# Kernel optimization log

Hardware: AMD Instinct MI355X
Metric: run time of the kernel (lower is better)

## Reference

```python
import jax, jax.numpy as jnp
import numpy as np

E = 65536            # total entities (flattened batch*history*slots)
ENTITY_SIZE = 256
NUM_SPECIES, NUM_ABILITIES, NUM_ITEMS, NUM_ACTIONS = 512, 128, 256, 512
# feature layout (column index in entity row)
SPECIES, ABILITY, ITEM = 0, 1, 2
SCALAR_FEATS = list(range(3, 16))   # level..fainted
SCALAR_MAX = [101, 2, 2, 32, 3, 8, 16, 2, 2, 2, 8, 4, 2]
BOOST_FEATS = list(range(16, 23))   # 7 boosts
BOOST_MAX = 13
VOL0, VOL8 = 23, 31                 # 9 uint16 volatile words
TC0, TC1 = 32, 33                   # 2 uint16 typechange words
MOVE0 = 34                          # 4 move-id tokens
NUM_FEATS = 38
HP_RATIO = 6
CONCAT_DIM = 512 + 128 + 256 + sum(SCALAR_MAX) + 7 * BOOST_MAX + 9 * 16 + 2 * 16 + 1  # = 1348

MAXES = np.ones(NUM_FEATS, dtype=np.int32)
MAXES[SPECIES], MAXES[ABILITY], MAXES[ITEM] = NUM_SPECIES, NUM_ABILITIES, NUM_ITEMS
for f, m in zip(SCALAR_FEATS, SCALAR_MAX):
    MAXES[f] = m
for f in BOOST_FEATS:
    MAXES[f] = BOOST_MAX
MAXES[VOL0:VOL8 + 1] = 65536
MAXES[TC0:TC1 + 1] = 65536
MAXES[MOVE0:MOVE0 + 4] = NUM_ACTIONS


def bits16(x):
    # x int32 [..., k] -> float bits [..., k*16]
    b = (x[..., None] >> jnp.arange(16, dtype=jnp.int32)) & 1
    return b.astype(jnp.float32).reshape(*x.shape[:-1], -1)


def setup_inputs() -> dict:
    key = jax.random.key(0)
    ks = jax.random.split(key, 12)
    u = jax.random.uniform(ks[0], (E, NUM_FEATS))
    entity = (u * jnp.asarray(MAXES, dtype=jnp.float32)).astype(jnp.int32)
    s = 0.02
    return {
        'entity': entity,
        'species_tbl': jax.random.normal(ks[1], (NUM_SPECIES, 512), jnp.float32) * s,
        'ability_tbl': jax.random.normal(ks[2], (NUM_ABILITIES, 128), jnp.float32) * s,
        'item_tbl': jax.random.normal(ks[3], (NUM_ITEMS, 256), jnp.float32) * s,
        'species_emb': jax.random.normal(ks[4], (NUM_SPECIES, ENTITY_SIZE), jnp.float32) * s,
        'ability_emb': jax.random.normal(ks[5], (NUM_ABILITIES, ENTITY_SIZE), jnp.float32) * s,
        'item_emb': jax.random.normal(ks[6], (NUM_ITEMS, ENTITY_SIZE), jnp.float32) * s,
        'actions_emb': jax.random.normal(ks[7], (NUM_ACTIONS, ENTITY_SIZE), jnp.float32) * s,
        'agg_w': jax.random.normal(ks[8], (CONCAT_DIM, ENTITY_SIZE), jnp.float32) * s,
        'agg_b': jnp.zeros((ENTITY_SIZE,), jnp.float32),
        'mlp_w': jax.random.normal(ks[9], (ENTITY_SIZE, ENTITY_SIZE), jnp.float32) * s,
        'mlp_b': jnp.zeros((ENTITY_SIZE,), jnp.float32),
    }


def reference(entity, species_tbl, ability_tbl, item_tbl, species_emb, ability_emb,
              item_emb, actions_emb, agg_w, agg_b, mlp_w, mlp_b):
    sp, ab, it = entity[:, SPECIES], entity[:, ABILITY], entity[:, ITEM]
    # pretrained one-hot / feature-table gathers
    enc = [species_tbl[sp], ability_tbl[ab], item_tbl[it]]
    # small scalar one-hots
    enc += [jax.nn.one_hot(entity[:, f], m, dtype=jnp.float32)
            for f, m in zip(SCALAR_FEATS, SCALAR_MAX)]
    # boost one-hots
    enc += [jax.nn.one_hot(entity[:, f], BOOST_MAX, dtype=jnp.float32) for f in BOOST_FEATS]
    # hex/binary encodings of volatile + typechange words
    enc.append(bits16(entity[:, VOL0:VOL8 + 1]))       # [E,144]
    enc.append(bits16(entity[:, TC0:TC1 + 1]))         # [E,32]
    # continuous feature (hp ratio)
    enc.append((entity[:, HP_RATIO].astype(jnp.float32) / 31.0)[:, None])
    concat = jnp.concatenate(enc, axis=-1)             # [E,1348]
    emb_sum = (species_emb[sp] + ability_emb[ab] + item_emb[it]
               + actions_emb[entity[:, MOVE0]] + actions_emb[entity[:, MOVE0 + 1]]
               + actions_emb[entity[:, MOVE0 + 2]] + actions_emb[entity[:, MOVE0 + 3]])
    x = concat @ agg_w + agg_b + emb_sum               # SumEmbeddings
    x = jax.nn.relu(x) @ mlp_w + mlp_b                 # MLP((entity_size,))
    mask = jnp.logical_and(sp != 0, sp != 1)           # not NULL / not PAD
    return jnp.where(mask[:, None], x, 0.0)
```

## Files before the change

### kernel.cpp

```cpp
#include <hip/hip_runtime.h>

#define NFEAT 38

typedef __attribute__((ext_vector_type(8))) short bf16x8;
typedef __attribute__((ext_vector_type(4))) float f32x4;
typedef __attribute__((ext_vector_type(2))) float f32x2;
typedef __attribute__((ext_vector_type(4))) unsigned int u32x4;

#define R_SP   0
#define R_AB   512
#define R_IT   640
#define R_T1   896
#define R_T2   1300
#define R_T3   1428
#define R_T4   1452
#define R_T5   1484
#define R_T6   1548
#define R_T7   1717
#define R_T8   1886
#define R_T9   2055
#define R_ACT  2068
#define NROWS  2580

#define B_FUSED  0
#define B_WMLP   112
#define B_WBITS  176
#define B_MERGED 224
#define B_IDXS   645
#define NB_PREP  709

__device__ __forceinline__ unsigned short f2bf(float f) {
    unsigned int u = __float_as_uint(f);
    u += 0x7fffu + ((u >> 16) & 1u);
    return (unsigned short)(u >> 16);
}

__device__ __forceinline__ unsigned int cvt_pk_bf16(float lo, float hi) {
    unsigned int r;
    asm("v_cvt_pk_bf16_f32 %0, %1, %2" : "=v"(r) : "v"(lo), "v"(hi));
    return r;
}

__global__ __launch_bounds__(1024) void k_prep(
    const float* __restrict__ sp_tbl, const float* __restrict__ ab_tbl,
    const float* __restrict__ it_tbl, const float* __restrict__ sp_emb,
    const float* __restrict__ ab_emb, const float* __restrict__ it_emb,
    const float* __restrict__ act_emb, const float* __restrict__ agg_w,
    const float* __restrict__ agg_b,  const float* __restrict__ mlp_w,
    const int* __restrict__ ent,
    unsigned short* __restrict__ tbl, unsigned short* __restrict__ wfrag,
    unsigned short* __restrict__ wbits, unsigned int* __restrict__ ridx)
{
    __shared__ float rowbuf[8 * 513];
    __shared__ float part[8][4][256];
    int blk = blockIdx.x, t = threadIdx.x, c = t & 255;
#define W(x) agg_w[(size_t)(x) * 256 + c]

    if (blk < B_WMLP) {
        int r0 = blk << 3;
        const float* src; const float* emb; int len, wbase, ls; bool add_b;
        if (r0 < 512)      { src = sp_tbl + (size_t)r0 * 512;           emb = sp_emb + (size_t)r0 * 256;           len = 512; ls = 9; wbase = 0;   add_b = true;  }
        else if (r0 < 640) { int q = r0 - 512; src = ab_tbl + (size_t)q * 128; emb = ab_emb + (size_t)q * 256; len = 128; ls = 7; wbase = 512; add_b = false; }
        else               { int q = r0 - 640; src = it_tbl + (size_t)q * 256; emb = it_emb + (size_t)q * 256; len = 256; ls = 8; wbase = 640; add_b = false; }
        int tot = len << 3;
        for (int i = t; i < tot; i += 1024)
            rowbuf[(i >> ls) * (len + 1) + (i & (len - 1))] = src[i];
        __syncthreads();
        int kq   = t >> 8;
        int len4 = len >> 2;
        int kbeg = kq * len4, kend = kbeg + len4;
        float a[8] = {0.f, 0.f, 0.f, 0.f, 0.f, 0.f, 0.f, 0.f};
        #pragma unroll 4
        for (int k = kbeg; k < kend; ++k) {
            float w = W(wbase + k);
            #pragma unroll
            for (int r = 0; r < 8; ++r) a[r] += rowbuf[r * (len + 1) + k] * w;
        }
        #pragma unroll
        for (int r = 0; r < 8; ++r) part[r][kq][c] = a[r];
        __syncthreads();
        int rr = t >> 8;
        #pragma unroll
        for (int h = 0; h < 2; ++h) {
            int row = rr + h * 4;
            float s = part[row][0][c] + part[row][1][c] + part[row][2][c] + part[row][3][c]
                    + emb[row * 256 + c] + (add_b ? agg_b[c] : 0.f);
            tbl[(size_t)(r0 + row) * 256 + c] = f2bf(s);
        }
        return;
    }
    if (blk < B_WBITS) {
        int idx = ((blk - B_WMLP) << 10) + t;
        int j   = idx & 7;
        int fl  = (idx >> 3) & 63;
        int k0g = (idx >> 9) & 7;
        int nt  = idx >> 12;
        int k   = k0g * 32 + (fl >> 4) * 8 + j;
        int col = nt * 16 + (fl & 15);
        wfrag[idx] = f2bf(mlp_w[(size_t)k * 256 + col]);
        return;
    }
    if (blk < B_MERGED) {
        int idx = ((blk - B_WBITS) << 10) + t;
        int j   = idx & 7;
        int ln  = (idx >> 3) & 63;
        int r2  = idx >> 9;
        int kt  = r2 % 6;
        int nt  = r2 / 6;
        int k   = kt * 32 + ((ln >> 4) << 3) + j;
        int col = (nt << 4) + (ln & 15);
        float v = (k < 176) ? agg_w[(size_t)(1171 + k) * 256 + col] : 0.f;
        wbits[idx] = f2bf(v);
        return;
    }
    if (blk < B_IDXS) {
        int r = ((blk - B_MERGED) << 2) + (t >> 8);
        int row; float acc;
        if (r < 404)       { int f3 = r >> 2, f4 = (r >> 1) & 1, f5 = r & 1;
                             acc = W(896 + f3) + W(997 + f4) + W(999 + f5); row = R_T1 + r; }
        else if (r < 532)  { int i = r - 404; int f6 = i >> 2, f11 = (i >> 1) & 1, f12 = i & 1;
                             acc = W(1001 + f6) + (float)f6 * (1.f / 31.f) * W(1347)
                                 + W(1062 + f11) + W(1064 + f12); row = R_T2 + i; }
        else if (r < 556)  { int i = r - 532; acc = W(1033 + (i >> 3)) + W(1036 + (i & 7)); row = R_T3 + i; }
        else if (r < 588)  { int i = r - 556; acc = W(1044 + (i >> 1)) + W(1060 + (i & 1)); row = R_T4 + i; }
        else if (r < 652)  { int i = r - 588; acc = W(1066 + (i >> 3)) + W(1074 + ((i >> 1) & 3)) + W(1078 + (i & 1)); row = R_T5 + i; }
        else if (r < 821)  { int i = r - 652; acc = W(1080 + i / 13) + W(1093 + i % 13); row = R_T6 + i; }
        else if (r < 990)  { int i = r - 821; acc = W(1106 + i / 13) + W(1119 + i % 13); row = R_T7 + i; }
        else if (r < 1159) { int i = r - 990; acc = W(1132 + i / 13) + W(1145 + i % 13); row = R_T8 + i; }
        else if (r < 1172) { int i = r - 1159; acc = W(1158 + i); row = R_T9 + i; }
        else               { int i = r - 1172; acc = act_emb[(size_t)i * 256 + c]; row = R_ACT + i; }
        tbl[(size_t)row * 256 + c] = f2bf(acc);
        return;
    }
    {
        int e = ((blk - B_IDXS) << 10) + t;
        size_t bb = (size_t)e * (NFEAT * 4);
        const uint4* wp = reinterpret_cast<const uint4*>(
            reinterpret_cast<const char*>(ent) + (bb & ~(size_t)15));
        uint4 q0 = wp[0], q1 = wp[1], q2 = wp[2], q3 = wp[3], q4 = wp[4];
        uint4 q5 = wp[5], q6 = wp[6], q7 = wp[7], q8 = wp[8], q9 = wp[9];
        unsigned int v[40] = {q0.x,q0.y,q0.z,q0.w, q1.x,q1.y,q1.z,q1.w,
                              q2.x,q2.y,q2.z,q2.w, q3.x,q3.y,q3.z,q3.w,
                              q4.x,q4.y,q4.z,q4.w, q5.x,q5.y,q5.z,q5.w,
                              q6.x,q6.y,q6.z,q6.w, q7.x,q7.y,q7.z,q7.w,
                              q8.x,q8.y,q8.z,q8.w, q9.x,q9.y,q9.z,q9.w};
        int f[NFEAT];
        if (e & 1) {
            #pragma unroll
            for (int i = 0; i < NFEAT; ++i) f[i] = (int)v[i + 2];
        } else {
            #pragma unroll
            for (int i = 0; i < NFEAT; ++i) f[i] = (int)v[i];
        }
        int rw[16];
        rw[0]  = f[0];
        rw[1]  = R_AB + f[1];
        rw[2]  = R_IT + f[2];
        rw[3]  = R_T1 + f[3] * 4 + f[4] * 2 + f[5];
        rw[4]  = R_T2 + f[6] * 4 + f[11] * 2 + f[12];
        rw[5]  = R_T3 + f[7] * 8 + f[8];
        rw[6]  = R_T4 + f[9] * 2 + f[10];
        rw[7]  = R_T5 + f[13] * 8 + f[14] * 2 + f[15];
        rw[8]  = R_T6 + f[16] * 13 + f[17];
        rw[9]  = R_T7 + f[18] * 13 + f[19];
        rw[10] = R_T8 + f[20] * 13 + f[21];
        rw[11] = R_T9 + f[22];
        rw[12] = R_ACT + f[34];
        rw[13] = R_ACT + f[35];
        rw[14] = R_ACT + f[36];
        rw[15] = R_ACT + f[37];
        unsigned int p[16];
        #pragma unroll
        for (int i = 0; i < 8; ++i)
            p[i] = (unsigned int)rw[2 * i] | ((unsigned int)rw[2 * i + 1] << 16);
        #pragma unroll
        for (int i = 0; i < 5; ++i)
            p[8 + i] = (unsigned int)(f[23 + 2 * i] & 0xffff) | ((unsigned int)f[24 + 2 * i] << 16);
        p[13] = (unsigned int)(f[33] & 0xffff);
        p[14] = 0; p[15] = 0;
        uint4* dst = reinterpret_cast<uint4*>(ridx + (size_t)e * 16);
        dst[0] = make_uint4(p[0], p[1], p[2], p[3]);
        dst[1] = make_uint4(p[4], p[5], p[6], p[7]);
        dst[2] = make_uint4(p[8], p[9], p[10], p[11]);
        dst[3] = make_uint4(p[12], p[13], p[14], p[15]);
    }
#undef W
}

__global__ __launch_bounds__(512, 4) void k_fused_em(
    const unsigned int* __restrict__ ridx, const unsigned short* __restrict__ tbl,
    const unsigned short* __restrict__ wfrag, const unsigned short* __restrict__ wbits,
    const float* __restrict__ mlp_b, float* __restrict__ out)
{
    __shared__ unsigned short xw[64 * 256];
    __shared__ unsigned int bitw[64 * 6];
    __shared__ unsigned char smask[64];
    int t    = threadIdx.x;
    int w    = t >> 6;
    int lane = t & 63;
    int half = lane >> 5;
    int cp   = lane & 31;
    int wu   = __builtin_amdgcn_readfirstlane(w);
    int eb   = blockIdx.x << 6;
    const char* tb = reinterpret_cast<const char*>(tbl);
    char* xb = reinterpret_cast<char*>(xw);

    if (t < 384) {
        int e = t / 6, k = t - e * 6;
        bitw[t] = ridx[(size_t)(eb + e) * 16 + 8 + k];
    }
    if (t < 64) smask[t] = ((ridx[(size_t)(eb + t) * 16] & 0xffffu) < 2u) ? 1 : 0;

    {
        int cb = cp << 4;
        int sh = half << 4;
        const unsigned int* rqw = ridx + (size_t)(eb + (wu << 3)) * 16;
        uint4 v[8], vn[8];
        #pragma unroll
        for (int j = 0; j < 8; ++j) {
            unsigned int pj = rqw[j];
            unsigned int row = (pj >> sh) & 0xffffu;
            v[j] = *reinterpret_cast<const uint4*>(tb + ((size_t)row << 9) + cb);
        }
        #pragma unroll
        for (int i = 0; i < 8; ++i) {
            if (i < 7) {
                const unsigned int* rq = rqw + ((i + 1) << 4);
                #pragma unroll
                for (int j = 0; j < 8; ++j) {
                    unsigned int pj = rq[j];
                    unsigned int row = (pj >> sh) & 0xffffu;
                    vn[j] = *reinterpret_cast<const uint4*>(tb + ((size_t)row << 9) + cb);
                }
            }
            int el = (wu << 3) + i;
            f32x2 aE0 = (f32x2){0.f, 0.f}, aO0 = (f32x2){0.f, 0.f};
            f32x2 aE1 = (f32x2){0.f, 0.f}, aO1 = (f32x2){0.f, 0.f};
            #pragma unroll
            for (int j = 0; j < 8; ++j) {
                aE0 += (f32x2){__uint_as_float(v[j].x << 16), __uint_as_float(v[j].y << 16)};
                aO0 += (f32x2){__uint_as_float(v[j].x),       __uint_as_float(v[j].y)};
                aE1 += (f32x2){__uint_as_float(v[j].z << 16), __uint_as_float(v[j].w << 16)};
                aO1 += (f32x2){__uint_as_float(v[j].z),       __uint_as_float(v[j].w)};
            }
            float s0 = aE0[0] + __shfl_xor(aE0[0], 32);
            float s1 = aO0[0] + __shfl_xor(aO0[0], 32);
            float s2 = aE0[1] + __shfl_xor(aE0[1], 32);
            float s3 = aO0[1] + __shfl_xor(aO0[1], 32);
            float s4 = aE1[0] + __shfl_xor(aE1[0], 32);
            float s5 = aO1[0] + __shfl_xor(aO1[0], 32);
            float s6 = aE1[1] + __shfl_xor(aE1[1], 32);
            float s7 = aO1[1] + __shfl_xor(aO1[1], 32);
            if (half == 0) {
                unsigned int o0 = cvt_pk_bf16(s0, s1);
                unsigned int o1 = cvt_pk_bf16(s2, s3);
                unsigned int o2 = cvt_pk_bf16(s4, s5);
                unsigned int o3 = cvt_pk_bf16(s6, s7);
                int up = cp ^ (el & 7);
                *reinterpret_cast<uint4*>(xb + (el << 9) + (up << 4)) = make_uint4(o0, o1, o2, o3);
            }
            #pragma unroll
            for (int j = 0; j < 8; ++j) v[j] = vn[j];
        }
    }
    __syncthreads();

    int rc  = lane & 15;
    int kg  = lane >> 4;
    int nt0 = wu << 1;
    int c0  = wu << 5;

    f32x4 D0[4], D1[4];
    #pragma unroll
    for (int mt = 0; mt < 4; ++mt) { D0[mt] = (f32x4){0.f,0.f,0.f,0.f}; D1[mt] = (f32x4){0.f,0.f,0.f,0.f}; }

    #pragma unroll
    for (int kt = 0; kt < 6; ++kt) {
        bf16x8 b0 = *reinterpret_cast<const bf16x8*>(wbits + (((size_t)(nt0 * 6 + kt)) << 9) + (lane << 3));
        bf16x8 b1 = *reinterpret_cast<const bf16x8*>(wbits + (((size_t)((nt0 + 1) * 6 + kt)) << 9) + (lane << 3));
        #pragma unroll
        for (int mt = 0; mt < 4; ++mt) {
            unsigned int wb = bitw[((mt << 4) + rc) * 6 + kt];
            unsigned int bs = wb >> (kg << 3);
            unsigned int e0 = ((bs & 1u)   ? 0x3F80u : 0u) | ((bs & 2u)   ? 0x3F800000u : 0u);
            unsigned int e1 = ((bs & 4u)   ? 0x3F80u : 0u) | ((bs & 8u)   ? 0x3F800000u : 0u);
            unsigned int e2 = ((bs & 16u)  ? 0x3F80u : 0u) | ((bs & 32u)  ? 0x3F800000u : 0u);
            unsigned int e3 = ((bs & 64u)  ? 0x3F80u : 0u) | ((bs & 128u) ? 0x3F800000u : 0u);
            bf16x8 afr = __builtin_bit_cast(bf16x8, (u32x4){e0, e1, e2, e3});
            D0[mt] = __builtin_amdgcn_mfma_f32_16x16x32_bf16(afr, b0, D0[mt], 0, 0, 0);
            D1[mt] = __builtin_amdgcn_mfma_f32_16x16x32_bf16(afr, b1, D1[mt], 0, 0, 0);
        }
    }

    #pragma unroll
    for (int mt = 0; mt < 4; ++mt) {
        #pragma unroll
        for (int j = 0; j < 4; ++j) {
            int row  = (mt << 4) + (kg << 2) + j;
            int colA = c0 + rc;
            int colB = colA + 16;
            int uA = (colA >> 3) ^ (row & 7);
            int uB = (colB >> 3) ^ (row & 7);
            unsigned short* pA = reinterpret_cast<unsigned short*>(
                xb + (row << 9) + (uA << 4) + ((colA & 7) << 1));
            unsigned short* pB = reinterpret_cast<unsigned short*>(
                xb + (row << 9) + (uB << 4) + ((colB & 7) << 1));
            float xA = __uint_as_float((unsigned int)(*pA) << 16) + D0[mt][j];
            float xB = __uint_as_float((unsigned int)(*pB) << 16) + D1[mt][j];
            *pA = (unsigned short)cvt_pk_bf16(fmaxf(xA, 0.f), 0.f);
            *pB = (unsigned short)cvt_pk_bf16(fmaxf(xB, 0.f), 0.f);
        }
    }
    __syncthreads();

    f32x4 acc0[4], acc1[4];
    #pragma unroll
    for (int mt = 0; mt < 4; ++mt) {
        acc0[mt] = (f32x4){0.f,0.f,0.f,0.f};
        acc1[mt] = (f32x4){0.f,0.f,0.f,0.f};
    }

    #pragma unroll
    for (int k0g = 0; k0g < 8; ++k0g) {
        bf16x8 b0 = *reinterpret_cast<const bf16x8*>(
            wfrag + (((size_t)(nt0 * 8 + k0g)) << 9) + (lane << 3));
        bf16x8 b1 = *reinterpret_cast<const bf16x8*>(
            wfrag + (((size_t)((nt0 + 1) * 8 + k0g)) << 9) + (lane << 3));
        int up = ((k0g << 2) + kg) ^ (rc & 7);
        #pragma unroll
        for (int mt = 0; mt < 4; ++mt) {
            int r = (mt << 4) + rc;
            bf16x8 a = *reinterpret_cast<const bf16x8*>(xb + (r << 9) + (up << 4));
            acc0[mt] = __builtin_amdgcn_mfma_f32_16x16x32_bf16(a, b0, acc0[mt], 0, 0, 0);
            acc1[mt] = __builtin_amdgcn_mfma_f32_16x16x32_bf16(a, b1, acc1[mt], 0, 0, 0);
        }
    }

    float bias0 = mlp_b[c0 + rc];
    float bias1 = mlp_b[c0 + 16 + rc];
    #pragma unroll
    for (int mt = 0; mt < 4; ++mt) {
        unsigned int mw = *reinterpret_cast<const unsigned int*>(&smask[(mt << 4) + (kg << 2)]);
        #pragma unroll
        for (int j = 0; j < 4; ++j) {
            int row = eb + (mt << 4) + (kg << 2) + j;
            bool m = (mw >> (8 * j)) & 1u;
            out[(size_t)row * 256 + c0 + rc]      = m ? 0.f : (acc0[mt][j] + bias0);
            out[(size_t)row * 256 + c0 + 16 + rc] = m ? 0.f : (acc1[mt][j] + bias1);
        }
    }
}

extern "C" void kernel_launch(void* const* d_in, const int* in_sizes, int n_in,
                              void* d_out, int out_size, void* d_ws, size_t ws_size,
                              hipStream_t stream)
{
    const int*   ent     = (const int*)d_in[0];
    const float* sp_tbl  = (const float*)d_in[1];
    const float* ab_tbl  = (const float*)d_in[2];
    const float* it_tbl  = (const float*)d_in[3];
    const float* sp_emb  = (const float*)d_in[4];
    const float* ab_emb  = (const float*)d_in[5];
    const float* it_emb  = (const float*)d_in[6];
    const float* act_emb = (const float*)d_in[7];
    const float* agg_w   = (const float*)d_in[8];
    const float* agg_b   = (const float*)d_in[9];
    const float* mlp_w   = (const float*)d_in[10];
    const float* mlp_b   = (const float*)d_in[11];
    float* out = (float*)d_out;

    char* ws = (char*)d_ws;
    unsigned short* tbl   = (unsigned short*)(ws);
    unsigned short* wfrag = (unsigned short*)(ws + 1320960);
    unsigned short* wbits = (unsigned short*)(ws + 1452032);
    unsigned int*   ridx  = (unsigned int*)  (ws + 1550336);

    k_prep    <<<dim3(NB_PREP), dim3(1024), 0, stream>>>(sp_tbl, ab_tbl, it_tbl,
                                                         sp_emb, ab_emb, it_emb,
                                                         act_emb, agg_w, agg_b, mlp_w,
                                                         ent, tbl, wfrag, wbits, ridx);
    k_fused_em<<<dim3(1024),    dim3(512),  0, stream>>>(ridx, tbl, wfrag, wbits, mlp_b, out);
}
```

Before: 70.74 us.

## Double-buffer table gathers with inline-asm loads and counted vmcnt waits

```diff
diff --git a/kernel.cpp b/kernel.cpp
--- a/kernel.cpp
+++ b/kernel.cpp
@@ -187,6 +187,55 @@
 #undef W
 }
 
+__device__ __forceinline__ void issue8(u32x4 (&bank)[8], const unsigned int* sw,
+                                       int sh, unsigned int cb, unsigned long long sbase)
+{
+    uint4 sx = *reinterpret_cast<const uint4*>(sw);
+    uint4 sy = *reinterpret_cast<const uint4*>(sw + 4);
+    unsigned int wv[8] = {sx.x, sx.y, sx.z, sx.w, sy.x, sy.y, sy.z, sy.w};
+    #pragma unroll
+    for (int j = 0; j < 8; ++j) {
+        unsigned int vo = (((wv[j] >> sh) & 0xffffu) << 9) + cb;
+        asm volatile("global_load_dwordx4 %0, %1, %2"
+                     : "=v"(bank[j]) : "v"(vo), "s"(sbase) : "memory");
+    }
+}
+
+__device__ __forceinline__ void consume8(const u32x4 (&v)[8], int el, int half,
+                                         int cp, char* xb)
+{
+    f32x2 aE0 = (f32x2){0.f, 0.f}, aO0 = (f32x2){0.f, 0.f};
+    f32x2 aE1 = (f32x2){0.f, 0.f}, aO1 = (f32x2){0.f, 0.f};
+    #pragma unroll
+    for (int j = 0; j < 8; ++j) {
+        aE0 += (f32x2){__uint_as_float(v[j][0] << 16), __uint_as_float(v[j][1] << 16)};
+        aO0 += (f32x2){__uint_as_float(v[j][0]),       __uint_as_float(v[j][1])};
+        aE1 += (f32x2){__uint_as_float(v[j][2] << 16), __uint_as_float(v[j][3] << 16)};
+        aO1 += (f32x2){__uint_as_float(v[j][2]),       __uint_as_float(v[j][3])};
+    }
+    float s0 = aE0[0] + __shfl_xor(aE0[0], 32);
+    float s1 = aO0[0] + __shfl_xor(aO0[0], 32);
+    float s2 = aE0[1] + __shfl_xor(aE0[1], 32);
+    float s3 = aO0[1] + __shfl_xor(aO0[1], 32);
+    float s4 = aE1[0] + __shfl_xor(aE1[0], 32);
+    float s5 = aO1[0] + __shfl_xor(aO1[0], 32);
+    float s6 = aE1[1] + __shfl_xor(aE1[1], 32);
+    float s7 = aO1[1] + __shfl_xor(aO1[1], 32);
+    if (half == 0) {
+        unsigned int o0 = cvt_pk_bf16(s0, s1);
+        unsigned int o1 = cvt_pk_bf16(s2, s3);
+        unsigned int o2 = cvt_pk_bf16(s4, s5);
+        unsigned int o3 = cvt_pk_bf16(s6, s7);
+        int up = cp ^ (el & 7);
+        *reinterpret_cast<uint4*>(xb + (el << 9) + (up << 4)) = make_uint4(o0, o1, o2, o3);
+    }
+}
+
+#define WAIT8 do { asm volatile("s_waitcnt vmcnt(8)" ::: "memory"); \
+                   __builtin_amdgcn_sched_barrier(0); } while (0)
+#define WAIT0 do { asm volatile("s_waitcnt vmcnt(0)" ::: "memory"); \
+                   __builtin_amdgcn_sched_barrier(0); } while (0)
+
 __global__ __launch_bounds__(512, 4) void k_fused_em(
     const unsigned int* __restrict__ ridx, const unsigned short* __restrict__ tbl,
     const unsigned short* __restrict__ wfrag, const unsigned short* __restrict__ wbits,
@@ -195,6 +244,7 @@
     __shared__ unsigned short xw[64 * 256];
     __shared__ unsigned int bitw[64 * 6];
     __shared__ unsigned char smask[64];
+    __shared__ unsigned int sids[64 * 8];
     int t    = threadIdx.x;
     int w    = t >> 6;
     int lane = t & 63;
@@ -205,6 +255,7 @@
     const char* tb = reinterpret_cast<const char*>(tbl);
     char* xb = reinterpret_cast<char*>(xw);
 
+    sids[t] = ridx[(size_t)(eb + (t >> 3)) * 16 + (t & 7)];
     if (t < 384) {
         int e = t / 6, k = t - e * 6;
         bitw[t] = ridx[(size_t)(eb + e) * 16 + 8 + k];
@@ -212,56 +263,22 @@
     if (t < 64) smask[t] = ((ridx[(size_t)(eb + t) * 16] & 0xffffu) < 2u) ? 1 : 0;
 
     {
-        int cb = cp << 4;
+        unsigned int cb = (unsigned int)(cp << 4);
         int sh = half << 4;
-        const unsigned int* rqw = ridx + (size_t)(eb + (wu << 3)) * 16;
-        uint4 v[8], vn[8];
-        #pragma unroll
-        for (int j = 0; j < 8; ++j) {
-            unsigned int pj = rqw[j];
-            unsigned int row = (pj >> sh) & 0xffffu;
-            v[j] = *reinterpret_cast<const uint4*>(tb + ((size_t)row << 9) + cb);
-        }
-        #pragma unroll
-        for (int i = 0; i < 8; ++i) {
-            if (i < 7) {
-                const unsigned int* rq = rqw + ((i + 1) << 4);
-                #pragma unroll
-                for (int j = 0; j < 8; ++j) {
-                    unsigned int pj = rq[j];
-                    unsigned int row = (pj >> sh) & 0xffffu;
-                    vn[j] = *reinterpret_cast<const uint4*>(tb + ((size_t)row << 9) + cb);
-                }
-            }
-            int el = (wu << 3) + i;
-            f32x2 aE0 = (f32x2){0.f, 0.f}, aO0 = (f32x2){0.f, 0.f};
-            f32x2 aE1 = (f32x2){0.f, 0.f}, aO1 = (f32x2){0.f, 0.f};
-            #pragma unroll
-            for (int j = 0; j < 8; ++j) {
-                aE0 += (f32x2){__uint_as_float(v[j].x << 16), __uint_as_float(v[j].y << 16)};
-                aO0 += (f32x2){__uint_as_float(v[j].x),       __uint_as_float(v[j].y)};
-                aE1 += (f32x2){__uint_as_float(v[j].z << 16), __uint_as_float(v[j].w << 16)};
-                aO1 += (f32x2){__uint_as_float(v[j].z),       __uint_as_float(v[j].w)};
-            }
-            float s0 = aE0[0] + __shfl_xor(aE0[0], 32);
-            float s1 = aO0[0] + __shfl_xor(aO0[0], 32);
-            float s2 = aE0[1] + __shfl_xor(aE0[1], 32);
-            float s3 = aO0[1] + __shfl_xor(aO0[1], 32);
-            float s4 = aE1[0] + __shfl_xor(aE1[0], 32);
-            float s5 = aO1[0] + __shfl_xor(aO1[0], 32);
-            float s6 = aE1[1] + __shfl_xor(aE1[1], 32);
-            float s7 = aO1[1] + __shfl_xor(aO1[1], 32);
-            if (half == 0) {
-                unsigned int o0 = cvt_pk_bf16(s0, s1);
-                unsigned int o1 = cvt_pk_bf16(s2, s3);
-                unsigned int o2 = cvt_pk_bf16(s4, s5);
-                unsigned int o3 = cvt_pk_bf16(s6, s7);
-                int up = cp ^ (el & 7);
-                *reinterpret_cast<uint4*>(xb + (el << 9) + (up << 4)) = make_uint4(o0, o1, o2, o3);
-            }
-            #pragma unroll
-            for (int j = 0; j < 8; ++j) v[j] = vn[j];
-        }
+        unsigned long long sbase = (unsigned long long)(const void*)tb;
+        const unsigned int* sw = sids + (wu << 6);
+        int e0l = wu << 3;
+        u32x4 bk0[8], bk1[8];
+        issue8(bk0, sw,      sh, cb, sbase);
+        issue8(bk1, sw + 8,  sh, cb, sbase);
+        WAIT8; consume8(bk0, e0l + 0, half, cp, xb); issue8(bk0, sw + 16, sh, cb, sbase);
+        WAIT8; consume8(bk1, e0l + 1, half, cp, xb); issue8(bk1, sw + 24, sh, cb, sbase);
+        WAIT8; consume8(bk0, e0l + 2, half, cp, xb); issue8(bk0, sw + 32, sh, cb, sbase);
+        WAIT8; consume8(bk1, e0l + 3, half, cp, xb); issue8(bk1, sw + 40, sh, cb, sbase);
+        WAIT8; consume8(bk0, e0l + 4, half, cp, xb); issue8(bk0, sw + 48, sh, cb, sbase);
+        WAIT8; consume8(bk1, e0l + 5, half, cp, xb); issue8(bk1, sw + 56, sh, cb, sbase);
+        WAIT8; consume8(bk0, e0l + 6, half, cp, xb);
+        WAIT0; consume8(bk1, e0l + 7, half, cp, xb);
     }
     __syncthreads();
 
```

Measured after the change: 70.12 us. Within noise of the previous version (-0.9%).

## Merge combo tables to 14 gathered rows and process two entities per wave

Applied to the files above, without the earlier changes.

```diff
diff --git a/kernel.cpp b/kernel.cpp
--- a/kernel.cpp
+++ b/kernel.cpp
@@ -11,23 +11,21 @@
 #define R_AB   512
 #define R_IT   640
 #define R_T1   896
-#define R_T2   1300
-#define R_T3   1428
-#define R_T4   1452
-#define R_T5   1484
-#define R_T6   1548
-#define R_T7   1717
-#define R_T8   1886
-#define R_T9   2055
-#define R_ACT  2068
-#define NROWS  2580
+#define R_T29  1300
+#define R_T34  2964
+#define R_T5   3732
+#define R_T6   3796
+#define R_T7   3965
+#define R_T8   4134
+#define R_ACT  4303
+#define NROWS  4815
 
 #define B_FUSED  0
 #define B_WMLP   112
 #define B_WBITS  176
 #define B_MERGED 224
-#define B_IDXS   645
-#define NB_PREP  709
+#define B_IDXS   1204
+#define NB_PREP  1268
 
 __device__ __forceinline__ unsigned short f2bf(float f) {
     unsigned int u = __float_as_uint(f);
@@ -115,21 +113,30 @@
     }
     if (blk < B_IDXS) {
         int r = ((blk - B_MERGED) << 2) + (t >> 8);
-        int row; float acc;
-        if (r < 404)       { int f3 = r >> 2, f4 = (r >> 1) & 1, f5 = r & 1;
-                             acc = W(896 + f3) + W(997 + f4) + W(999 + f5); row = R_T1 + r; }
-        else if (r < 532)  { int i = r - 404; int f6 = i >> 2, f11 = (i >> 1) & 1, f12 = i & 1;
-                             acc = W(1001 + f6) + (float)f6 * (1.f / 31.f) * W(1347)
-                                 + W(1062 + f11) + W(1064 + f12); row = R_T2 + i; }
-        else if (r < 556)  { int i = r - 532; acc = W(1033 + (i >> 3)) + W(1036 + (i & 7)); row = R_T3 + i; }
-        else if (r < 588)  { int i = r - 556; acc = W(1044 + (i >> 1)) + W(1060 + (i & 1)); row = R_T4 + i; }
-        else if (r < 652)  { int i = r - 588; acc = W(1066 + (i >> 3)) + W(1074 + ((i >> 1) & 3)) + W(1078 + (i & 1)); row = R_T5 + i; }
-        else if (r < 821)  { int i = r - 652; acc = W(1080 + i / 13) + W(1093 + i % 13); row = R_T6 + i; }
-        else if (r < 990)  { int i = r - 821; acc = W(1106 + i / 13) + W(1119 + i % 13); row = R_T7 + i; }
-        else if (r < 1159) { int i = r - 990; acc = W(1132 + i / 13) + W(1145 + i % 13); row = R_T8 + i; }
-        else if (r < 1172) { int i = r - 1159; acc = W(1158 + i); row = R_T9 + i; }
-        else               { int i = r - 1172; acc = act_emb[(size_t)i * 256 + c]; row = R_ACT + i; }
-        tbl[(size_t)row * 256 + c] = f2bf(acc);
+        if (r < 3919) {
+            int row; float acc;
+            if (r < 404)       { int f3 = r >> 2, f4 = (r >> 1) & 1, f5 = r & 1;
+                                 acc = W(896 + f3) + W(997 + f4) + W(999 + f5); row = R_T1 + r; }
+            else if (r < 2068) { int i = r - 404; int t2 = i / 13, f22 = i % 13;
+                                 int f6 = t2 >> 2, f11 = (t2 >> 1) & 1, f12 = t2 & 1;
+                                 acc = W(1001 + f6) + (float)f6 * (1.f / 31.f) * W(1347)
+                                     + W(1062 + f11) + W(1064 + f12) + W(1158 + f22);
+                                 row = R_T29 + i; }
+            else if (r < 2836) { int i = r - 2068; int f78 = i >> 5;
+                                 acc = W(1033 + (f78 >> 3)) + W(1036 + (f78 & 7))
+                                     + W(1044 + ((i >> 1) & 15)) + W(1060 + (i & 1));
+                                 row = R_T34 + i; }
+            else if (r < 2900) { int i = r - 2836;
+                                 acc = W(1066 + (i >> 3)) + W(1074 + ((i >> 1) & 3)) + W(1078 + (i & 1));
+                                 row = R_T5 + i; }
+            else if (r < 3407) { int i = r - 2900;
+                                 if (i < 169)      { acc = W(1080 + i / 13) + W(1093 + i % 13); row = R_T6 + i; }
+                                 else if (i < 338) { int q = i - 169; acc = W(1106 + q / 13) + W(1119 + q % 13); row = R_T7 + q; }
+                                 else              { int q = i - 338; acc = W(1132 + q / 13) + W(1145 + q % 13); row = R_T8 + q; }
+                               }
+            else               { int i = r - 3407; acc = act_emb[(size_t)i * 256 + c]; row = R_ACT + i; }
+            tbl[(size_t)row * 256 + c] = f2bf(acc);
+        }
         return;
     }
     {
@@ -152,27 +159,26 @@
             #pragma unroll
             for (int i = 0; i < NFEAT; ++i) f[i] = (int)v[i];
         }
-        int rw[16];
+        int rw[14];
         rw[0]  = f[0];
         rw[1]  = R_AB + f[1];
         rw[2]  = R_IT + f[2];
         rw[3]  = R_T1 + f[3] * 4 + f[4] * 2 + f[5];
-        rw[4]  = R_T2 + f[6] * 4 + f[11] * 2 + f[12];
-        rw[5]  = R_T3 + f[7] * 8 + f[8];
-        rw[6]  = R_T4 + f[9] * 2 + f[10];
-        rw[7]  = R_T5 + f[13] * 8 + f[14] * 2 + f[15];
-        rw[8]  = R_T6 + f[16] * 13 + f[17];
-        rw[9]  = R_T7 + f[18] * 13 + f[19];
-        rw[10] = R_T8 + f[20] * 13 + f[21];
-        rw[11] = R_T9 + f[22];
-        rw[12] = R_ACT + f[34];
-        rw[13] = R_ACT + f[35];
-        rw[14] = R_ACT + f[36];
-        rw[15] = R_ACT + f[37];
+        rw[4]  = R_T29 + (f[6] * 4 + f[11] * 2 + f[12]) * 13 + f[22];
+        rw[5]  = R_T34 + (f[7] * 8 + f[8]) * 32 + f[9] * 2 + f[10];
+        rw[6]  = R_T5 + f[13] * 8 + f[14] * 2 + f[15];
+        rw[7]  = R_T6 + f[16] * 13 + f[17];
+        rw[8]  = R_T7 + f[18] * 13 + f[19];
+        rw[9]  = R_T8 + f[20] * 13 + f[21];
+        rw[10] = R_ACT + f[34];
+        rw[11] = R_ACT + f[35];
+        rw[12] = R_ACT + f[36];
+        rw[13] = R_ACT + f[37];
         unsigned int p[16];
         #pragma unroll
-        for (int i = 0; i < 8; ++i)
+        for (int i = 0; i < 7; ++i)
             p[i] = (unsigned int)rw[2 * i] | ((unsigned int)rw[2 * i + 1] << 16);
+        p[7] = (unsigned int)f[0];
         #pragma unroll
         for (int i = 0; i < 5; ++i)
             p[8 + i] = (unsigned int)(f[23 + 2 * i] & 0xffff) | ((unsigned int)f[24 + 2 * i] << 16);
@@ -195,6 +201,7 @@
     __shared__ unsigned short xw[64 * 256];
     __shared__ unsigned int bitw[64 * 6];
     __shared__ unsigned char smask[64];
+    __shared__ unsigned int sids[64 * 8];
     int t    = threadIdx.x;
     int w    = t >> 6;
     int lane = t & 63;
@@ -205,62 +212,63 @@
     const char* tb = reinterpret_cast<const char*>(tbl);
     char* xb = reinterpret_cast<char*>(xw);
 
+    sids[t] = ridx[(size_t)(eb + (t >> 3)) * 16 + (t & 7)];
     if (t < 384) {
         int e = t / 6, k = t - e * 6;
         bitw[t] = ridx[(size_t)(eb + e) * 16 + 8 + k];
     }
-    if (t < 64) smask[t] = ((ridx[(size_t)(eb + t) * 16] & 0xffffu) < 2u) ? 1 : 0;
+    if (t < 64) smask[t] = (ridx[(size_t)(eb + t) * 16 + 7] < 2u) ? 1 : 0;
 
     {
-        int cb = cp << 4;
-        int sh = half << 4;
-        const unsigned int* rqw = ridx + (size_t)(eb + (wu << 3)) * 16;
-        uint4 v[8], vn[8];
-        #pragma unroll
-        for (int j = 0; j < 8; ++j) {
-            unsigned int pj = rqw[j];
-            unsigned int row = (pj >> sh) & 0xffffu;
-            v[j] = *reinterpret_cast<const uint4*>(tb + ((size_t)row << 9) + cb);
-        }
-        #pragma unroll
-        for (int i = 0; i < 8; ++i) {
-            if (i < 7) {
-                const unsigned int* rq = rqw + ((i + 1) << 4);
+        unsigned int cb = (unsigned int)(cp << 4);
+        const unsigned int* sw = sids + (wu << 6);
+        unsigned int rr[14], rn[14];
+        uint4 v[14], vn[14];
+
+        auto rows_of = [&](int p, unsigned int (&dst)[14]) {
+            const unsigned int* wp = sw + (((p << 1) + half) << 3);
+            uint4 wa = *reinterpret_cast<const uint4*>(wp);
+            uint4 wb = *reinterpret_cast<const uint4*>(wp + 4);
+            dst[0]  = wa.x & 0xffffu; dst[1]  = wa.x >> 16;
+            dst[2]  = wa.y & 0xffffu; dst[3]  = wa.y >> 16;
+            dst[4]  = wa.z & 0xffffu; dst[5]  = wa.z >> 16;
+            dst[6]  = wa.w & 0xffffu; dst[7]  = wa.w >> 16;
+            dst[8]  = wb.x & 0xffffu; dst[9]  = wb.x >> 16;
+            dst[10] = wb.y & 0xffffu; dst[11] = wb.y >> 16;
+            dst[12] = wb.z & 0xffffu; dst[13] = wb.z >> 16;
+        };
+
+        rows_of(0, rr);
+        #pragma unroll
+        for (int j = 0; j < 14; ++j)
+            v[j] = *reinterpret_cast<const uint4*>(tb + ((size_t)rr[j] << 9) + cb);
+
+        #pragma unroll
+        for (int p = 0; p < 4; ++p) {
+            if (p < 3) {
+                rows_of(p + 1, rn);
                 #pragma unroll
-                for (int j = 0; j < 8; ++j) {
-                    unsigned int pj = rq[j];
-                    unsigned int row = (pj >> sh) & 0xffffu;
-                    vn[j] = *reinterpret_cast<const uint4*>(tb + ((size_t)row << 9) + cb);
-                }
+                for (int j = 0; j < 14; ++j)
+                    vn[j] = *reinterpret_cast<const uint4*>(tb + ((size_t)rn[j] << 9) + cb);
             }
-            int el = (wu << 3) + i;
             f32x2 aE0 = (f32x2){0.f, 0.f}, aO0 = (f32x2){0.f, 0.f};
             f32x2 aE1 = (f32x2){0.f, 0.f}, aO1 = (f32x2){0.f, 0.f};
             #pragma unroll
-            for (int j = 0; j < 8; ++j) {
+            for (int j = 0; j < 14; ++j) {
                 aE0 += (f32x2){__uint_as_float(v[j].x << 16), __uint_as_float(v[j].y << 16)};
                 aO0 += (f32x2){__uint_as_float(v[j].x),       __uint_as_float(v[j].y)};
                 aE1 += (f32x2){__uint_as_float(v[j].z << 16), __uint_as_float(v[j].w << 16)};
                 aO1 += (f32x2){__uint_as_float(v[j].z),       __uint_as_float(v[j].w)};
             }
-            float s0 = aE0[0] + __shfl_xor(aE0[0], 32);
-            float s1 = aO0[0] + __shfl_xor(aO0[0], 32);
-            float s2 = aE0[1] + __shfl_xor(aE0[1], 32);
-            float s3 = aO0[1] + __shfl_xor(aO0[1], 32);
-            float s4 = aE1[0] + __shfl_xor(aE1[0], 32);
-            float s5 = aO1[0] + __shfl_xor(aO1[0], 32);
-            float s6 = aE1[1] + __shfl_xor(aE1[1], 32);
-            float s7 = aO1[1] + __shfl_xor(aO1[1], 32);
-            if (half == 0) {
-                unsigned int o0 = cvt_pk_bf16(s0, s1);
-                unsigned int o1 = cvt_pk_bf16(s2, s3);
-                unsigned int o2 = cvt_pk_bf16(s4, s5);
-                unsigned int o3 = cvt_pk_bf16(s6, s7);
-                int up = cp ^ (el & 7);
-                *reinterpret_cast<uint4*>(xb + (el << 9) + (up << 4)) = make_uint4(o0, o1, o2, o3);
-            }
-            #pragma unroll
-            for (int j = 0; j < 8; ++j) v[j] = vn[j];
+            unsigned int o0 = cvt_pk_bf16(aE0[0], aO0[0]);
+            unsigned int o1 = cvt_pk_bf16(aE0[1], aO0[1]);
+            unsigned int o2 = cvt_pk_bf16(aE1[0], aO1[0]);
+            unsigned int o3 = cvt_pk_bf16(aE1[1], aO1[1]);
+            int el = (wu << 3) + (p << 1) + half;
+            int up = cp ^ (el & 7);
+            *reinterpret_cast<uint4*>(xb + (el << 9) + (up << 4)) = make_uint4(o0, o1, o2, o3);
+            #pragma unroll
+            for (int j = 0; j < 14; ++j) v[j] = vn[j];
         }
     }
     __syncthreads();
@@ -371,9 +379,9 @@
 
     char* ws = (char*)d_ws;
     unsigned short* tbl   = (unsigned short*)(ws);
-    unsigned short* wfrag = (unsigned short*)(ws + 1320960);
-    unsigned short* wbits = (unsigned short*)(ws + 1452032);
-    unsigned int*   ridx  = (unsigned int*)  (ws + 1550336);
+    unsigned short* wfrag = (unsigned short*)(ws + 2465280);
+    unsigned short* wbits = (unsigned short*)(ws + 2596352);
+    unsigned int*   ridx  = (unsigned int*)  (ws + 2694656);
 
     k_prep    <<<dim3(NB_PREP), dim3(1024), 0, stream>>>(sp_tbl, ab_tbl, it_tbl,
                                                          sp_emb, ab_emb, it_emb,
```

New measurement: 70.32 us. No clear change (-0.6%).
